# Kernel optimization log

Hardware: AMD Instinct MI355X
Metric: run time of the kernel (lower is better)

The kernel has to match this reference:

```python
import jax, jax.numpy as jnp
import numpy as np

HIDDEN = 2048
HEADS = 16
HEAD_DIM = HIDDEN // HEADS
BATCH = 2
SEQ = 2048


def setup_inputs() -> dict:
    key = jax.random.key(0)
    ks = jax.random.split(key, 9)
    s = 0.02
    return {
        "x": jax.random.normal(ks[0], (BATCH, SEQ, HIDDEN), dtype=jnp.float32),
        "wq": jax.random.normal(ks[1], (HIDDEN, HIDDEN), dtype=jnp.float32) * s,
        "bq": jax.random.normal(ks[2], (HIDDEN,), dtype=jnp.float32) * s,
        "wk": jax.random.normal(ks[3], (HIDDEN, HIDDEN), dtype=jnp.float32) * s,
        "bk": jax.random.normal(ks[4], (HIDDEN,), dtype=jnp.float32) * s,
        "wv": jax.random.normal(ks[5], (HIDDEN, HIDDEN), dtype=jnp.float32) * s,
        "bv": jax.random.normal(ks[6], (HIDDEN,), dtype=jnp.float32) * s,
        "wo": jax.random.normal(ks[7], (HIDDEN, HIDDEN), dtype=jnp.float32) * s,
        "bo": jax.random.normal(ks[8], (HIDDEN,), dtype=jnp.float32) * s,
    }


def reference(x, wq, bq, wk, bk, wv, bv, wo, bo):
    B, S, _ = x.shape
    scale = jnp.sqrt(jnp.float32(HEAD_DIM))
    # torch Linear: y = x @ W.T + b
    def proj(w, b):
        return (x @ w.T + b).reshape(B, S, HEADS, HEAD_DIM).transpose(0, 2, 1, 3)
    q = proj(wq, bq)  # [B,H,S,D]
    k = proj(wk, bk)
    v = proj(wv, bv)
    scores = jnp.einsum("bhqd,bhkd->bhqk", q, k) / scale  # [B,H,S,S]
    probs = jax.nn.softmax(scores, axis=-1)
    ctx = jnp.einsum("bhqk,bhkd->bhqd", probs, v)  # [B,H,S,D]
    ctx = ctx.transpose(0, 2, 1, 3).reshape(B, S, HIDDEN)
    return ctx @ wo.T + bo
```

## Files before the change

kernel.cpp:

```cpp
#include <hip/hip_runtime.h>

typedef unsigned short u16;
typedef unsigned int   u32;
typedef float  f32x4   __attribute__((ext_vector_type(4)));
typedef __bf16 bf16x8  __attribute__((ext_vector_type(8)));
typedef u16    u16x8   __attribute__((ext_vector_type(8)));
typedef u16    u16x4   __attribute__((ext_vector_type(4)));
typedef u32    u32x2   __attribute__((ext_vector_type(2)));
typedef u32    u32x4   __attribute__((ext_vector_type(4)));

#define HIDDEN 2048
#define SEQ    2048
#define NHEADS 16
#define HD     128
#define BATCH  2
#define QSTR   4096

typedef const __attribute__((address_space(3))) u16* lptr;

__device__ __forceinline__ u16 f2bf(float f) {
  u32 u = __builtin_bit_cast(u32, f);
  u += 0x7FFFu + ((u >> 16) & 1u);
  return (u16)(u >> 16);
}
__device__ __forceinline__ u32 pk2(float a, float b) {
  __bf16 x = (__bf16)a, y = (__bf16)b;
  return (u32)__builtin_bit_cast(u16, x) | ((u32)__builtin_bit_cast(u16, y) << 16);
}
__device__ __forceinline__ bf16x8 ld_frag(const u16* p) {
  return __builtin_bit_cast(bf16x8, *(const u32x4*)p);
}
__device__ __forceinline__ void gload_lds16(const u16* g, u16* l) {
  __builtin_amdgcn_global_load_lds((const __attribute__((address_space(1))) u32*)g,
                                   (__attribute__((address_space(3))) u32*)l, 16, 0, 0);
}

#define DSR(dst, base, lit) \
  asm volatile("ds_read_b128 %0, %1 offset:" lit : "=v"(dst) : "v"(base))

__global__ __launch_bounds__(256) void cvt_kernel(const float* __restrict__ src,
                                                  u16* __restrict__ dst, int n4) {
  int stride = gridDim.x * blockDim.x;
  for (int i = blockIdx.x * blockDim.x + threadIdx.x; i < n4; i += stride) {
    f32x4 v = ((const f32x4*)src)[i];
    u16x4 o;
    o[0] = f2bf(v[0]); o[1] = f2bf(v[1]); o[2] = f2bf(v[2]); o[3] = f2bf(v[3]);
    *(u16x4*)(dst + (size_t)i * 4) = o;
  }
}

__global__ __launch_bounds__(256) void cvt4_kernel(
    const float* __restrict__ s0, const float* __restrict__ s1,
    const float* __restrict__ s2, const float* __restrict__ s3,
    u16* __restrict__ o0, u16* __restrict__ o1,
    u16* __restrict__ o2, u16* __restrict__ o3, int n4) {
  const float* src = (blockIdx.y == 0) ? s0 : (blockIdx.y == 1) ? s1 : (blockIdx.y == 2) ? s2 : s3;
  u16* dst = (blockIdx.y == 0) ? o0 : (blockIdx.y == 1) ? o1 : (blockIdx.y == 2) ? o2 : o3;
  int stride = gridDim.x * blockDim.x;
  for (int i = blockIdx.x * blockDim.x + threadIdx.x; i < n4; i += stride) {
    f32x4 v = ((const f32x4*)src)[i];
    u16x4 o;
    o[0] = f2bf(v[0]); o[1] = f2bf(v[1]); o[2] = f2bf(v[2]); o[3] = f2bf(v[3]);
    *(u16x4*)(dst + (size_t)i * 4) = o;
  }
}

__global__ __launch_bounds__(512, 2) void gemm_qkv(
    const u16* __restrict__ A, const u16* __restrict__ Bt,
    const float* __restrict__ bq, const float* __restrict__ bk,
    const float* __restrict__ bv,
    u16* __restrict__ qk, u16* __restrict__ vtb, float qscale)
{
  __shared__ __attribute__((aligned(16))) u16 As[2][16384];
  __shared__ __attribute__((aligned(16))) u16 Bs[2][12288];

  const int tid  = threadIdx.x;
  const int lane = tid & 63;
  const int wave = tid >> 6;
  const int l15  = lane & 15;
  const int g    = lane >> 4;
  const int wm   = wave >> 2;
  const int wn   = wave & 3;

  const int id  = blockIdx.x;
  const int xcd = id & 7;
  const int c   = id >> 3;
  const int tileN = (xcd * 4 + (c >> 4)) * 192;
  const int tileM = (c & 15) << 8;

  const int srow = tid >> 3;
  const int gch8 = ((tid & 7) ^ (srow & 7)) * 8;
  const u16* agp = A  + (size_t)(tileM + srow) * HIDDEN + gch8;
  const u16* bgp = Bt + (size_t)(tileN + srow) * HIDDEN + gch8;
  u16* asp = (u16*)&As[0][0] + tid * 8;
  u16* bsp = (u16*)&Bs[0][0] + tid * 8;

  auto stage = [&](int buf, int ko) {
    u16* ad = asp + buf * 16384;
    u16* bd = bsp + buf * 12288;
#pragma unroll
    for (int r = 0; r < 4; ++r)
      gload_lds16(agp + (size_t)r * 64 * HIDDEN + ko, ad + r * 4096);
#pragma unroll
    for (int r = 0; r < 3; ++r)
      gload_lds16(bgp + (size_t)r * 64 * HIDDEN + ko, bd + r * 4096);
  };

  const int sw = l15 & 7;
  const int c0 = (g ^ sw) * 8;
  const int c1 = ((g ^ sw) ^ 4) * 8;
  lptr aT = (lptr)&As[0][0] + (size_t)(wm * 128 + l15) * 64;
  lptr bT = (lptr)&Bs[0][0] + (size_t)(wn * 48 + l15) * 64;

  f32x4 acc[8][3] = {};
  bf16x8 Xa[8], Xb[3], Ya[8], Yb[3];

#define ISSUE_SET(Sa, Sb, ab, bb)      \
  DSR(Sa[0], ab, "0");                 \
  DSR(Sa[1], ab, "2048");              \
  DSR(Sa[2], ab, "4096");              \
  DSR(Sa[3], ab, "6144");              \
  DSR(Sa[4], ab, "8192");              \
  DSR(Sa[5], ab, "10240");             \
  DSR(Sa[6], ab, "12288");             \
  DSR(Sa[7], ab, "14336");             \
  DSR(Sb[0], bb, "0");                 \
  DSR(Sb[1], bb, "2048");              \
  DSR(Sb[2], bb, "4096");

#define MFMA24(Sa, Sb)                                                                    \
  _Pragma("unroll")                                                                       \
  for (int mf = 0; mf < 8; ++mf) {                                                        \
    _Pragma("unroll")                                                                     \
    for (int nf = 0; nf < 3; ++nf)                                                        \
      acc[mf][nf] = __builtin_amdgcn_mfma_f32_16x16x32_bf16(Sa[mf], Sb[nf], acc[mf][nf], 0, 0, 0); \
  }

  stage(0, 0);
  stage(1, 64);
  asm volatile("s_waitcnt vmcnt(7)" ::: "memory");
  __builtin_amdgcn_s_barrier();
  __builtin_amdgcn_sched_barrier(0);
  {
    lptr ab = aT + c0;
    lptr bb = bT + c0;
    ISSUE_SET(Xa, Xb, ab, bb)
  }

#pragma unroll 2
  for (int t = 0; t < 32; ++t) {
    const int cur = t & 1;
    lptr aC = aT + cur * 16384;
    lptr bC = bT + cur * 12288;
    {
      lptr ab = aC + c1;
      lptr bb = bC + c1;
      ISSUE_SET(Ya, Yb, ab, bb)
    }
    asm volatile("s_waitcnt lgkmcnt(11)" ::: "memory");
    __builtin_amdgcn_sched_barrier(0);
    __builtin_amdgcn_s_setprio(1);
    MFMA24(Xa, Xb)
    __builtin_amdgcn_s_setprio(0);
    asm volatile("s_waitcnt lgkmcnt(0)" ::: "memory");
    __builtin_amdgcn_sched_barrier(0);
    __builtin_amdgcn_s_setprio(1);
    MFMA24(Ya, Yb)
    __builtin_amdgcn_s_setprio(0);
    __builtin_amdgcn_s_barrier();
    __builtin_amdgcn_sched_barrier(0);
    if (t < 30) {
      stage(cur, (t + 2) * 64);
      asm volatile("s_waitcnt vmcnt(7)" ::: "memory");
    } else {
      asm volatile("s_waitcnt vmcnt(0)" ::: "memory");
    }
    __builtin_amdgcn_s_barrier();
    __builtin_amdgcn_sched_barrier(0);
    if (t < 31) {
      lptr ab = aT + (cur ^ 1) * 16384 + c0;
      lptr bb = bT + (cur ^ 1) * 12288 + c0;
      ISSUE_SET(Xa, Xb, ab, bb)
    }
  }

#pragma unroll
  for (int mi = 0; mi < 8; ++mi) {
#pragma unroll
    for (int ni = 0; ni < 3; ++ni) {
      const int gcb = tileN + wn * 48 + ni * 16;
      const int seg = gcb >> 11;
      const int gc  = gcb + l15;
      const float bvv = ((seg == 0) ? bq : (seg == 1) ? bk : bv)[gc & 2047];
      if (seg < 2) {
        const float scl = (seg == 0) ? qscale : 1.f;
#pragma unroll
        for (int j = 0; j < 4; ++j) {
          const int gr = tileM + wm * 128 + mi * 16 + g * 4 + j;
          qk[(size_t)gr * QSTR + gc] = f2bf((acc[mi][ni][j] + bvv) * scl);
        }
      } else {
        const int dglob = gc - 4096;
        const int hh = dglob >> 7, dd = dglob & 127;
        const int srow0 = tileM + wm * 128 + mi * 16 + g * 4;
        const int bb = srow0 >> 11, ss = srow0 & 2047;
        u16x4 o;
#pragma unroll
        for (int j = 0; j < 4; ++j) o[j] = f2bf(acc[mi][ni][j] + bvv);
        *(u16x4*)(vtb + ((size_t)((bb * NHEADS + hh) * HD + dd)) * SEQ + ss) = o;
      }
    }
  }
#undef ISSUE_SET
#undef MFMA24
}

__global__ __launch_bounds__(256, 2) void gemm_bt(
    const u16* __restrict__ A, const u16* __restrict__ Bt,
    const float* __restrict__ bias, float* __restrict__ Cout,
    int M, int N, int K)
{
  __shared__ __attribute__((aligned(16))) u16 As[128 * 32];
  __shared__ __attribute__((aligned(16))) u16 Bs[128 * 32];
  const int tid  = threadIdx.x;
  const int lane = tid & 63;
  const int wave = tid >> 6;

  const int nbx   = N >> 7;
  const int nby   = M >> 7;
  const int id    = blockIdx.x;
  const int xcd   = id & 7;
  const int c     = id >> 3;
  const int cpx   = nbx >> 3;
  const int tileN = (xcd * cpx + c / nby) << 7;
  const int tileM = (c % nby) << 7;

  const int g = lane >> 4, r = lane & 15;

  const int srow = lane >> 2;
  const int scol = (lane & 3) * 8;
  const u16* ag0 = A  + (size_t)(tileM + wave * 16 + srow) * K + scol;
  const u16* ag1 = ag0 + (size_t)64 * K;
  const u16* bg0 = Bt + (size_t)(tileN + wave * 16 + srow) * K + scol;
  const u16* bg1 = bg0 + (size_t)64 * K;
  u16* as0 = &As[wave * 512];
  u16* as1 = &As[(wave + 4) * 512];
  u16* bs0 = &Bs[wave * 512];
  u16* bs1 = &Bs[(wave + 4) * 512];

  const int wm = wave >> 1, wn = wave & 1;
  const u16* afp = &As[(wm * 64 + r) * 32 + g * 8];
  const u16* bfp = &Bs[(wn * 64 + r) * 32 + g * 8];

  f32x4 acc[4][4] = {};

  for (int kt = 0; kt < K; kt += 32) {
    __syncthreads();
    gload_lds16(ag0 + kt, as0);
    gload_lds16(ag1 + kt, as1);
    gload_lds16(bg0 + kt, bs0);
    gload_lds16(bg1 + kt, bs1);
    __syncthreads();
    bf16x8 af[4], bf[4];
#pragma unroll
    for (int mi = 0; mi < 4; mi++) af[mi] = ld_frag(afp + mi * 512);
#pragma unroll
    for (int ni = 0; ni < 4; ni++) bf[ni] = ld_frag(bfp + ni * 512);
#pragma unroll
    for (int mi = 0; mi < 4; mi++)
#pragma unroll
      for (int ni = 0; ni < 4; ni++)
        acc[mi][ni] = __builtin_amdgcn_mfma_f32_16x16x32_bf16(af[mi], bf[ni], acc[mi][ni], 0, 0, 0);
  }

#pragma unroll
  for (int mi = 0; mi < 4; mi++) {
#pragma unroll
    for (int ni = 0; ni < 4; ni++) {
      const int gc = tileN + wn * 64 + ni * 16 + r;
      const float bv = bias[gc];
#pragma unroll
      for (int j = 0; j < 4; j++) {
        const int gr = tileM + wm * 64 + mi * 16 + g * 4 + j;
        Cout[(size_t)gr * N + gc] = acc[mi][ni][j] + bv;
      }
    }
  }
}

__global__ __launch_bounds__(256, 4) void attn_kernel(
    const u16* __restrict__ QKg, const u16* __restrict__ Vtg, u16* __restrict__ Ctx)
{
  __shared__ __attribute__((aligned(16))) u16 Ks[2][32 * 128];
  __shared__ __attribute__((aligned(16))) u16 Vs[2][128 * 32];

  const int tid  = threadIdx.x;
  const int lane = tid & 63;
  const int wave = tid >> 6;
  const int g4   = lane >> 4;
  const int l15  = lane & 15;

  const int wg = ((blockIdx.x & 7) << 7) + (blockIdx.x >> 3);
  const int bh = wg >> 5;
  const int qt = wg & 31;
  const int b  = bh >> 4, h = bh & 15;

  const u16* Qb  = QKg + (size_t)b * SEQ * QSTR + (size_t)h * HD;
  const u16* Kb  = Qb + 2048;
  const u16* Vth = Vtg + (size_t)bh * HD * SEQ;
  u16* Cb = Ctx + (size_t)b * SEQ * HIDDEN + (size_t)h * HD;

  const int qbase = qt * 64 + wave * 16 + l15;

  bf16x8 qf[4];
#pragma unroll
  for (int dc = 0; dc < 4; dc++)
    qf[dc] = ld_frag(Qb + (size_t)qbase * QSTR + dc * 32 + g4 * 8);

  const int kvp0 = (l15 >> 2) * 8 + (l15 & 3);
  const int msw  = (l15 & 3) | (((l15 >> 2) & 1) << 2);
  const int vch  = (g4 ^ (l15 >> 2)) * 8;

  f32x4 ctx[8] = {};
  float m_run = -1e30f;
  float l_run = 0.f;

  auto stage = [&](int buf, int kv0) {
#pragma unroll
    for (int i = 0; i < 2; i++) {
      const int idx = tid + i * 256;
      const int kv = idx >> 4, up = idx & 15;
      const int um = up ^ ((kv & 3) | (((kv >> 3) & 1) << 2));
      gload_lds16(Kb + (size_t)(kv0 + kv) * QSTR + um * 8, &Ks[buf][idx * 8]);
      const int d = idx >> 2, u = idx & 3;
      const int uv = u ^ ((d >> 2) & 3);
      gload_lds16(Vth + (size_t)d * SEQ + kv0 + uv * 8, &Vs[buf][idx * 8]);
    }
  };

  stage(0, 0);
  __syncthreads();

  const int NT = SEQ / 32;
  for (int t = 0; t < NT; t++) {
    const int buf = t & 1;
    if (t + 1 < NT) stage(buf ^ 1, (t + 1) * 32);

    f32x4 s[2] = {};
    __builtin_amdgcn_s_setprio(1);
#pragma unroll
    for (int ni = 0; ni < 2; ni++) {
      const int row = kvp0 + ni * 4;
#pragma unroll
      for (int dc = 0; dc < 4; dc++) {
        bf16x8 kf = ld_frag(&Ks[buf][row * 128 + (((dc * 4 + g4) ^ msw) * 8)]);
        s[ni] = __builtin_amdgcn_mfma_f32_16x16x32_bf16(kf, qf[dc], s[ni], 0, 0, 0);
      }
    }
    __builtin_amdgcn_s_setprio(0);

    float pmax = fmaxf(fmaxf(fmaxf(s[0][0], s[0][1]), fmaxf(s[0][2], s[0][3])),
                       fmaxf(fmaxf(s[1][0], s[1][1]), fmaxf(s[1][2], s[1][3])));
    pmax = fmaxf(pmax, __shfl_xor(pmax, 16));
    pmax = fmaxf(pmax, __shfl_xor(pmax, 32));
    if (!__all(pmax <= m_run + 8.f)) {
      const float mn = fmaxf(m_run, pmax);
      const float corr = exp2f(m_run - mn);
      m_run = mn;
      l_run *= corr;
#pragma unroll
      for (int dt = 0; dt < 8; dt++)
#pragma unroll
        for (int j = 0; j < 4; j++) ctx[dt][j] *= corr;
    }
    float ps = 0.f;
#pragma unroll
    for (int ni = 0; ni < 2; ni++)
#pragma unroll
      for (int j = 0; j < 4; j++) {
        const float p = exp2f(s[ni][j] - m_run);
        s[ni][j] = p;
        ps += p;
      }
    ps += __shfl_xor(ps, 16);
    ps += __shfl_xor(ps, 32);
    l_run += ps;
    u32x4 pw;
    pw[0] = pk2(s[0][0], s[0][1]);
    pw[1] = pk2(s[0][2], s[0][3]);
    pw[2] = pk2(s[1][0], s[1][1]);
    pw[3] = pk2(s[1][2], s[1][3]);
    const bf16x8 pfrag = __builtin_bit_cast(bf16x8, pw);

    __builtin_amdgcn_s_setprio(1);
#pragma unroll
    for (int dt = 0; dt < 8; dt++) {
      bf16x8 vf = ld_frag(&Vs[buf][(dt * 16 + l15) * 32 + vch]);
      ctx[dt] = __builtin_amdgcn_mfma_f32_16x16x32_bf16(vf, pfrag, ctx[dt], 0, 0, 0);
    }
    __builtin_amdgcn_s_setprio(0);

    __syncthreads();
  }

  const float linv = 1.f / l_run;
  u16* crow = Cb + (size_t)qbase * HIDDEN;
#pragma unroll
  for (int dt = 0; dt < 8; dt++) {
    u16x4 o;
#pragma unroll
    for (int j = 0; j < 4; j++) o[j] = f2bf(ctx[dt][j] * linv);
    *(u16x4*)&crow[dt * 16 + g4 * 4] = o;
  }
}

extern "C" void kernel_launch(void* const* d_in, const int* in_sizes, int n_in,
                              void* d_out, int out_size, void* d_ws, size_t ws_size,
                              hipStream_t stream) {
  (void)in_sizes; (void)n_in; (void)out_size; (void)ws_size;
  const float* x  = (const float*)d_in[0];
  const float* wq = (const float*)d_in[1];
  const float* bq = (const float*)d_in[2];
  const float* wk = (const float*)d_in[3];
  const float* bk = (const float*)d_in[4];
  const float* wv = (const float*)d_in[5];
  const float* bv = (const float*)d_in[6];
  const float* wo = (const float*)d_in[7];
  const float* bo = (const float*)d_in[8];

  const size_t NX = (size_t)BATCH * SEQ * HIDDEN;
  const size_t NW = (size_t)HIDDEN * HIDDEN;
  u16* xb   = (u16*)d_ws;
  u16* wqb  = xb  + NX;
  u16* wkb  = wqb + NW;
  u16* wvb  = wkb + NW;
  u16* wob  = wvb + NW;
  u16* qk   = wob + NW;
  u16* vtb  = qk  + 2 * NX;
  u16* ctxb = xb;

  cvt_kernel<<<2048, 256, 0, stream>>>(x, xb, (int)(NX / 4));
  cvt4_kernel<<<dim3(512, 4), 256, 0, stream>>>(wq, wk, wv, wo, wqb, wkb, wvb, wob, (int)(NW / 4));

  const float qscale = 0.12751744174240807f;
  gemm_qkv<<<512, 512, 0, stream>>>(xb, wqb, bq, bk, bv, qk, vtb, qscale);

  attn_kernel<<<1024, 256, 0, stream>>>(qk, vtb, ctxb);

  gemm_bt<<<512, 256, 0, stream>>>(ctxb, wob, bo, (float*)d_out, BATCH * SEQ, HIDDEN, HIDDEN);
}
```

Measured before the change: 289.6 us.

## Hand-schedule attention LDS reads and MFMAs with explicit waitcnts and barriers

Rewrites the attention inner loop to issue all K and V fragment LDS reads up front with inline ds_read_b128 and fixed offsets, then interleaves MFMAs with partial lgkmcnt waits. Global-to-LDS staging now uses an explicit vmcnt wait plus raw s_barrier instead of __syncthreads, so the next tile's loads are allowed to stay in flight. Launch bounds drop from 4 to 3 waves per SIMD to give more registers for the preloaded fragments. This trades occupancy and scheduler freedom for tighter latency hiding, and relies on hand-set wait counts being correct.

New measurement: 287.9 us. About the same (-0.6%).

```diff
diff --git a/kernel.cpp b/kernel.cpp
--- a/kernel.cpp
+++ b/kernel.cpp
@@ -37,6 +37,8 @@
 
 #define DSR(dst, base, lit) \
   asm volatile("ds_read_b128 %0, %1 offset:" lit : "=v"(dst) : "v"(base))
+
+#define MFMA16(d, a, b) d = __builtin_amdgcn_mfma_f32_16x16x32_bf16(a, b, d, 0, 0, 0)
 
 __global__ __launch_bounds__(256) void cvt_kernel(const float* __restrict__ src,
                                                   u16* __restrict__ dst, int n4) {
@@ -288,7 +290,7 @@
   }
 }
 
-__global__ __launch_bounds__(256, 4) void attn_kernel(
+__global__ __launch_bounds__(256, 3) void attn_kernel(
     const u16* __restrict__ QKg, const u16* __restrict__ Vtg, u16* __restrict__ Ctx)
 {
   __shared__ __attribute__((aligned(16))) u16 Ks[2][32 * 128];
@@ -319,7 +321,13 @@
 
   const int kvp0 = (l15 >> 2) * 8 + (l15 & 3);
   const int msw  = (l15 & 3) | (((l15 >> 2) & 1) << 2);
-  const int vch  = (g4 ^ (l15 >> 2)) * 8;
+
+  lptr kB = (lptr)&Ks[0][0] + kvp0 * 128;
+  lptr kb0 = kB + (((0 * 4 + g4) ^ msw) * 8);
+  lptr kb1 = kB + (((1 * 4 + g4) ^ msw) * 8);
+  lptr kb2 = kB + (((2 * 4 + g4) ^ msw) * 8);
+  lptr kb3 = kB + (((3 * 4 + g4) ^ msw) * 8);
+  lptr vb0 = (lptr)&Vs[0][0] + l15 * 32 + ((g4 ^ (l15 >> 2)) * 8);
 
   f32x4 ctx[8] = {};
   float m_run = -1e30f;
@@ -339,28 +347,49 @@
   };
 
   stage(0, 0);
-  __syncthreads();
 
   const int NT = SEQ / 32;
   for (int t = 0; t < NT; t++) {
     const int buf = t & 1;
-    if (t + 1 < NT) stage(buf ^ 1, (t + 1) * 32);
-
-    f32x4 s[2] = {};
+
+    if (t + 1 < NT) {
+      stage(buf ^ 1, (t + 1) * 32);
+      asm volatile("s_waitcnt vmcnt(4)" ::: "memory");
+    } else {
+      asm volatile("s_waitcnt vmcnt(0)" ::: "memory");
+    }
+    __builtin_amdgcn_s_barrier();
+    __builtin_amdgcn_sched_barrier(0);
+
+    bf16x8 k0, k1, k2, k3, k4, k5, k6, k7;
+    {
+      const int bo = buf * 4096;
+      lptr a0 = kb0 + bo, a1 = kb1 + bo, a2 = kb2 + bo, a3 = kb3 + bo;
+      DSR(k0, a0, "0");
+      DSR(k1, a1, "0");
+      DSR(k2, a2, "0");
+      DSR(k3, a3, "0");
+      DSR(k4, a0, "1024");
+      DSR(k5, a1, "1024");
+      DSR(k6, a2, "1024");
+      DSR(k7, a3, "1024");
+    }
+    f32x4 s0 = {}, s1 = {};
+    asm volatile("s_waitcnt lgkmcnt(4)" ::: "memory");
+    __builtin_amdgcn_sched_barrier(0);
     __builtin_amdgcn_s_setprio(1);
-#pragma unroll
-    for (int ni = 0; ni < 2; ni++) {
-      const int row = kvp0 + ni * 4;
-#pragma unroll
-      for (int dc = 0; dc < 4; dc++) {
-        bf16x8 kf = ld_frag(&Ks[buf][row * 128 + (((dc * 4 + g4) ^ msw) * 8)]);
-        s[ni] = __builtin_amdgcn_mfma_f32_16x16x32_bf16(kf, qf[dc], s[ni], 0, 0, 0);
-      }
-    }
+    MFMA16(s0, k0, qf[0]); MFMA16(s0, k1, qf[1]);
+    MFMA16(s0, k2, qf[2]); MFMA16(s0, k3, qf[3]);
+    __builtin_amdgcn_sched_barrier(0);
+    asm volatile("s_waitcnt lgkmcnt(0)" ::: "memory");
+    __builtin_amdgcn_sched_barrier(0);
+    MFMA16(s1, k4, qf[0]); MFMA16(s1, k5, qf[1]);
+    MFMA16(s1, k6, qf[2]); MFMA16(s1, k7, qf[3]);
     __builtin_amdgcn_s_setprio(0);
-
-    float pmax = fmaxf(fmaxf(fmaxf(s[0][0], s[0][1]), fmaxf(s[0][2], s[0][3])),
-                       fmaxf(fmaxf(s[1][0], s[1][1]), fmaxf(s[1][2], s[1][3])));
+    __builtin_amdgcn_sched_barrier(0);
+
+    float pmax = fmaxf(fmaxf(fmaxf(s0[0], s0[1]), fmaxf(s0[2], s0[3])),
+                       fmaxf(fmaxf(s1[0], s1[1]), fmaxf(s1[2], s1[3])));
     pmax = fmaxf(pmax, __shfl_xor(pmax, 16));
     pmax = fmaxf(pmax, __shfl_xor(pmax, 32));
     if (!__all(pmax <= m_run + 8.f)) {
@@ -375,32 +404,49 @@
     }
     float ps = 0.f;
 #pragma unroll
-    for (int ni = 0; ni < 2; ni++)
-#pragma unroll
-      for (int j = 0; j < 4; j++) {
-        const float p = exp2f(s[ni][j] - m_run);
-        s[ni][j] = p;
-        ps += p;
-      }
+    for (int j = 0; j < 4; j++) {
+      s0[j] = exp2f(s0[j] - m_run);
+      s1[j] = exp2f(s1[j] - m_run);
+      ps += s0[j] + s1[j];
+    }
     ps += __shfl_xor(ps, 16);
     ps += __shfl_xor(ps, 32);
     l_run += ps;
     u32x4 pw;
-    pw[0] = pk2(s[0][0], s[0][1]);
-    pw[1] = pk2(s[0][2], s[0][3]);
-    pw[2] = pk2(s[1][0], s[1][1]);
-    pw[3] = pk2(s[1][2], s[1][3]);
+    pw[0] = pk2(s0[0], s0[1]);
+    pw[1] = pk2(s0[2], s0[3]);
+    pw[2] = pk2(s1[0], s1[1]);
+    pw[3] = pk2(s1[2], s1[3]);
     const bf16x8 pfrag = __builtin_bit_cast(bf16x8, pw);
-
+    __builtin_amdgcn_sched_barrier(0);
+
+    bf16x8 v0, v1, v2, v3, v4, v5, v6, v7;
+    {
+      lptr vB = vb0 + buf * 4096;
+      DSR(v0, vB, "0");
+      DSR(v1, vB, "1024");
+      DSR(v2, vB, "2048");
+      DSR(v3, vB, "3072");
+      DSR(v4, vB, "4096");
+      DSR(v5, vB, "5120");
+      DSR(v6, vB, "6144");
+      DSR(v7, vB, "7168");
+    }
+    asm volatile("s_waitcnt lgkmcnt(4)" ::: "memory");
+    __builtin_amdgcn_sched_barrier(0);
     __builtin_amdgcn_s_setprio(1);
-#pragma unroll
-    for (int dt = 0; dt < 8; dt++) {
-      bf16x8 vf = ld_frag(&Vs[buf][(dt * 16 + l15) * 32 + vch]);
-      ctx[dt] = __builtin_amdgcn_mfma_f32_16x16x32_bf16(vf, pfrag, ctx[dt], 0, 0, 0);
-    }
+    MFMA16(ctx[0], v0, pfrag); MFMA16(ctx[1], v1, pfrag);
+    MFMA16(ctx[2], v2, pfrag); MFMA16(ctx[3], v3, pfrag);
+    __builtin_amdgcn_sched_barrier(0);
+    asm volatile("s_waitcnt lgkmcnt(0)" ::: "memory");
+    __builtin_amdgcn_sched_barrier(0);
+    MFMA16(ctx[4], v4, pfrag); MFMA16(ctx[5], v5, pfrag);
+    MFMA16(ctx[6], v6, pfrag); MFMA16(ctx[7], v7, pfrag);
     __builtin_amdgcn_s_setprio(0);
-
-    __syncthreads();
+    __builtin_amdgcn_sched_barrier(0);
+
+    __builtin_amdgcn_s_barrier();
+    __builtin_amdgcn_sched_barrier(0);
   }
 
   const float linv = 1.f / l_run;
```
